# Kernel optimization log

Hardware: AMD Instinct MI355X
Metric: run time of the kernel (lower is better)

## Reference

```python
import jax, jax.numpy as jnp
import numpy as np

NATTRS, NOBJS = 200, 500
N = NATTRS + NOBJS
E = 50000
IN_F, HID, NODE_D = 512, 2048, 512
IMG_D, EMB = 512, 800
B = 256


def _ln(x, g, b, eps=1e-5):
    mu = jnp.mean(x, axis=-1, keepdims=True)
    var = jnp.mean((x - mu) ** 2, axis=-1, keepdims=True)
    return (x - mu) * jax.lax.rsqrt(var + eps) * g + b


def _sage(x, src, dst, Wl, bl, Wr):
    # PyG SAGEConv: lin_l(mean_{j->i} x_j) + lin_r(x_i); lin_r has no bias.
    agg = jax.ops.segment_sum(x[src], dst, num_segments=x.shape[0])
    cnt = jax.ops.segment_sum(jnp.ones((src.shape[0],), x.dtype), dst, num_segments=x.shape[0])
    mean = agg / jnp.maximum(cnt, 1.0)[:, None]
    return mean @ Wl + bl + x @ Wr


def setup_inputs() -> dict:
    key = jax.random.key(0)
    ks = iter(jax.random.split(key, 40))
    rn = lambda shape, s=0.02: jax.random.normal(next(ks), shape, jnp.float32) * s
    inp = dict(
        img=jax.random.normal(next(ks), (B, IMG_D), jnp.float32),
        node_feats=jax.random.normal(next(ks), (N, IN_F), jnp.float32),
        edge_index=jax.random.randint(next(ks), (2, E), 0, N),
        # SAGEConv 1: in_f -> 2048
        s1_Wl=rn((IN_F, HID)), s1_bl=jnp.zeros((HID,), jnp.float32), s1_Wr=rn((IN_F, HID)),
        # SAGEConv 2: 2048 -> node_dim
        s2_Wl=rn((HID, NODE_D)), s2_bl=jnp.zeros((NODE_D,), jnp.float32), s2_Wr=rn((HID, NODE_D)),
        # img_fc: 512 -> 800 -> 1000 -> 800 (LayerNorm+ReLU hidden, LayerNorm output)
        i_W1=rn((IMG_D, 800)), i_b1=jnp.zeros((800,), jnp.float32), i_g1=jnp.ones((800,), jnp.float32), i_be1=jnp.zeros((800,), jnp.float32),
        i_W2=rn((800, 1000)), i_b2=jnp.zeros((1000,), jnp.float32), i_g2=jnp.ones((1000,), jnp.float32), i_be2=jnp.zeros((1000,), jnp.float32),
        i_W3=rn((1000, EMB)), i_b3=jnp.zeros((EMB,), jnp.float32), i_gn=jnp.ones((EMB,), jnp.float32), i_bn=jnp.zeros((EMB,), jnp.float32),
        # pair_fc: 1024 -> 1000 -> 800
        p_W1=rn((2 * NODE_D, 1000)), p_b1=jnp.zeros((1000,), jnp.float32), p_g1=jnp.ones((1000,), jnp.float32), p_be1=jnp.zeros((1000,), jnp.float32),
        p_W2=rn((1000, EMB)), p_b2=jnp.zeros((EMB,), jnp.float32), p_gn=jnp.ones((EMB,), jnp.float32), p_bn=jnp.zeros((EMB,), jnp.float32),
    )
    return inp


def reference(img, node_feats, edge_index,
              s1_Wl, s1_bl, s1_Wr, s2_Wl, s2_bl, s2_Wr,
              i_W1, i_b1, i_g1, i_be1, i_W2, i_b2, i_g2, i_be2, i_W3, i_b3, i_gn, i_bn,
              p_W1, p_b1, p_g1, p_be1, p_W2, p_b2, p_gn, p_bn):
    src, dst = edge_index[0], edge_index[1]
    # GAE.encode: SAGE -> ReLU -> (Dropout, eval=id) -> SAGE
    h = jax.nn.relu(_sage(node_feats, src, dst, s1_Wl, s1_bl, s1_Wr))
    nodes = _sage(h, src, dst, s2_Wl, s2_bl, s2_Wr)  # [N, node_dim]
    # img_fc
    t = jax.nn.relu(_ln(img @ i_W1 + i_b1, i_g1, i_be1))
    t = jax.nn.relu(_ln(t @ i_W2 + i_b2, i_g2, i_be2))
    img_feats = _ln(t @ i_W3 + i_b3, i_gn, i_bn)  # [B, EMB]
    # get_all_pairs (open-world cross product: attr repeated per obj, obj tiled)
    attr_nodes, obj_nodes = nodes[:NATTRS], nodes[NATTRS:]
    pairs = jnp.concatenate(
        [jnp.repeat(attr_nodes, NOBJS, axis=0), jnp.tile(obj_nodes, (NATTRS, 1))], axis=1)  # [P, 2*node_dim]
    u = jax.nn.relu(_ln(pairs @ p_W1 + p_b1, p_g1, p_be1))
    pair_nodes = _ln(u @ p_W2 + p_b2, p_gn, p_bn)  # [P, EMB]
    pair_pred = img_feats @ pair_nodes.T  # [B, P]
    return pair_pred, nodes
```

## Files before the change

### kernel.cpp

```cpp
#include <hip/hip_runtime.h>
#include <hip/hip_bf16.h>

#define NATTRS 200
#define NOBJS  500
#define NNODE  700
#define IN_F   512
#define HID    2048
#define NODE_D 512
#define IMG_D  512
#define EMB    800
#define BB     256
#define P_H1   1000
#define NPAIR  100000

typedef __attribute__((ext_vector_type(8))) short short8v;
typedef __attribute__((ext_vector_type(4))) float f32x4;

typedef const __attribute__((address_space(1))) unsigned int* gas_ptr;
typedef __attribute__((address_space(3))) unsigned int* las_ptr;
__device__ __forceinline__ void async_copy16(void* lds, const void* g) {
  __builtin_amdgcn_global_load_lds((gas_ptr)g, (las_ptr)lds, 16, 0, 0);
}

__device__ __forceinline__ ushort f2bf(float x) {
  __hip_bfloat16 b = __float2bfloat16(x);
  return *reinterpret_cast<ushort*>(&b);
}
__device__ __forceinline__ float bf2f(ushort u) {
  __hip_bfloat16 b;
  *reinterpret_cast<ushort*>(&b) = u;
  return __bfloat162float(b);
}

__global__ void k_count(const int* __restrict__ ei, int* __restrict__ cnt, int E) {
  int e = blockIdx.x * 256 + threadIdx.x;
  if (e < E) atomicAdd(&cnt[ei[E + e]], 1);
}

__global__ __launch_bounds__(1024) void k_scan(const int* __restrict__ cnt,
                                               int* __restrict__ row_start,
                                               int* __restrict__ pos) {
  __shared__ int s[1024];
  int t = threadIdx.x;
  int my = (t < NNODE) ? cnt[t] : 0;
  s[t] = my;
  __syncthreads();
  for (int off = 1; off < 1024; off <<= 1) {
    int add = (t >= off) ? s[t - off] : 0;
    __syncthreads();
    s[t] += add;
    __syncthreads();
  }
  int excl = s[t] - my;
  if (t < NNODE) { row_start[t] = excl; pos[t] = excl; }
  if (t == 0) row_start[NNODE] = s[1023];
}

__global__ void k_fill(const int* __restrict__ ei, int* __restrict__ pos,
                       int* __restrict__ srcs, int E) {
  int e = blockIdx.x * 256 + threadIdx.x;
  if (e < E) {
    int d = ei[E + e];
    int idx = atomicAdd(&pos[d], 1);
    srcs[idx] = ei[e];
  }
}

__global__ __launch_bounds__(256) void agg_mean(const float* __restrict__ X,
                                                const int* __restrict__ srcs,
                                                const int* __restrict__ row_start,
                                                float* __restrict__ outp, int D) {
  int node = blockIdx.x;
  int d = blockIdx.y * 256 + threadIdx.x;
  int e0 = row_start[node], e1 = row_start[node + 1];
  float s = 0.f;
  for (int e = e0; e < e1; ++e) s += X[srcs[e] * D + d];
  float c = (float)(e1 - e0);
  outp[node * D + d] = s / fmaxf(c, 1.f);
}

__global__ __launch_bounds__(256) void split_f32(const float* __restrict__ X,
                                                 ushort* __restrict__ Xh,
                                                 ushort* __restrict__ Xl,
                                                 int Mvalid, int K, int Kpad, long total) {
  for (long idx = blockIdx.x * 256L + threadIdx.x; idx < total; idx += gridDim.x * 256L) {
    int m = (int)(idx / Kpad);
    int k = (int)(idx - (long)m * Kpad);
    float v = (m < Mvalid && k < K) ? X[(size_t)m * K + k] : 0.f;
    ushort h = f2bf(v);
    Xh[idx] = h;
    Xl[idx] = f2bf(v - bf2f(h));
  }
}

__global__ __launch_bounds__(256) void prep_wT(const float* __restrict__ W,
                                               ushort* __restrict__ Wh,
                                               ushort* __restrict__ Wl,
                                               int K, int N, int Kpad) {
  __shared__ float tile[32][33];
  const int n0 = blockIdx.x * 32, k0 = blockIdx.y * 32;
  const int tx = threadIdx.x & 31, ty = threadIdx.x >> 5;
  #pragma unroll
  for (int r0 = 0; r0 < 32; r0 += 8) {
    int k = k0 + r0 + ty, n = n0 + tx;
    tile[r0 + ty][tx] = (k < K && n < N) ? W[(size_t)k * N + n] : 0.f;
  }
  __syncthreads();
  #pragma unroll
  for (int r0 = 0; r0 < 32; r0 += 8) {
    int n = n0 + r0 + ty, kk = k0 + tx;
    float v = tile[tx][r0 + ty];
    ushort h = f2bf(v);
    Wh[(size_t)n * Kpad + kk] = h;
    Wl[(size_t)n * Kpad + kk] = f2bf(v - bf2f(h));
  }
}

template <bool RELU>
__global__ __launch_bounds__(256) void ln_rows(float* __restrict__ X,
                                               const float* __restrict__ g,
                                               const float* __restrict__ b, int N) {
  int row = blockIdx.x, tid = threadIdx.x;
  float* x = X + row * N;
  float s1 = 0.f, s2 = 0.f;
  for (int i = tid; i < N; i += 256) { float v = x[i]; s1 += v; s2 += v * v; }
  #pragma unroll
  for (int m = 1; m < 64; m <<= 1) { s1 += __shfl_xor(s1, m); s2 += __shfl_xor(s2, m); }
  __shared__ float r1[4], r2[4];
  int wv = tid >> 6;
  if ((tid & 63) == 0) { r1[wv] = s1; r2[wv] = s2; }
  __syncthreads();
  s1 = r1[0] + r1[1] + r1[2] + r1[3];
  s2 = r2[0] + r2[1] + r2[2] + r2[3];
  float inv = 1.f / (float)N;
  float mu = s1 * inv;
  float rstd = rsqrtf(s2 * inv - mu * mu + 1e-5f);
  for (int i = tid; i < N; i += 256) {
    float v = (x[i] - mu) * rstd * g[i] + b[i];
    if (RELU) v = fmaxf(v, 0.f);
    x[i] = v;
  }
}

__global__ __launch_bounds__(256) void prep_img(const float* __restrict__ t3,
                                                ushort* __restrict__ ih,
                                                ushort* __restrict__ il) {
  int r = blockIdx.x;
  for (int n = threadIdx.x; n < EMB; n += 256) {
    float v = t3[r * EMB + n];
    ushort h = f2bf(v);
    ih[r * EMB + n] = h;
    il[r * EMB + n] = f2bf(v - bf2f(h));
  }
}

__global__ __launch_bounds__(256) void ugen(const float* __restrict__ B1v,
                                            const float* __restrict__ O1v,
                                            const float* __restrict__ g1,
                                            const float* __restrict__ be1,
                                            ushort* __restrict__ Uh,
                                            ushort* __restrict__ Ul, int p0) {
  int r = blockIdx.x * 4 + (threadIdx.x >> 6);
  int lane = threadIdx.x & 63;
  int p = p0 + r;
  if (p > NPAIR - 1) p = NPAIR - 1;
  int a = p / NOBJS, o = p - a * NOBJS;
  const float* br = B1v + a * P_H1;
  const float* ow = O1v + o * P_H1;
  float x[16];
  float s1 = 0.f, s2 = 0.f;
  #pragma unroll
  for (int i = 0; i < 16; ++i) {
    int k = lane + 64 * i;
    float v = 0.f;
    if (k < P_H1) v = br[k] + ow[k];
    x[i] = v; s1 += v; s2 += v * v;
  }
  #pragma unroll
  for (int m = 1; m < 64; m <<= 1) { s1 += __shfl_xor(s1, m); s2 += __shfl_xor(s2, m); }
  float mu = s1 * (1.f / P_H1);
  float rstd = rsqrtf(s2 * (1.f / P_H1) - mu * mu + 1e-5f);
  size_t rb = (size_t)r * 1024;
  #pragma unroll
  for (int i = 0; i < 16; ++i) {
    int k = lane + 64 * i;
    float un = 0.f;
    if (k < P_H1) un = fmaxf((x[i] - mu) * rstd * g1[k] + be1[k], 0.f);
    ushort h = f2bf(un);
    Uh[rb + k] = h;
    Ul[rb + k] = f2bf(un - bf2f(h));
  }
}

__global__ __launch_bounds__(256) void ln2k(const float* __restrict__ Vr,
                                            const float* __restrict__ gn,
                                            const float* __restrict__ bn,
                                            ushort* __restrict__ Vh,
                                            ushort* __restrict__ Vl) {
  int r = blockIdx.x * 4 + (threadIdx.x >> 6);
  int lane = threadIdx.x & 63;
  const float* row = Vr + (size_t)r * EMB;
  float x[13];
  float s1 = 0.f, s2 = 0.f;
  #pragma unroll
  for (int i = 0; i < 13; ++i) {
    int k = lane + 64 * i;
    float v = (k < EMB) ? row[k] : 0.f;
    x[i] = v; s1 += v; s2 += v * v;
  }
  #pragma unroll
  for (int m = 1; m < 64; m <<= 1) { s1 += __shfl_xor(s1, m); s2 += __shfl_xor(s2, m); }
  float mu = s1 * (1.f / EMB);
  float rstd = rsqrtf(s2 * (1.f / EMB) - mu * mu + 1e-5f);
  size_t rb = (size_t)r * EMB;
  #pragma unroll
  for (int i = 0; i < 13; ++i) {
    int k = lane + 64 * i;
    if (k < EMB) {
      float v = (x[i] - mu) * rstd * gn[k] + bn[k];
      ushort h = f2bf(v);
      Vh[rb + k] = h;
      Vl[rb + k] = f2bf(v - bf2f(h));
    }
  }
}

template <bool HAS2, bool HASBIAS, bool RELU>
__global__ __launch_bounds__(256, 3) void gemm_mf(
    const ushort* __restrict__ Ah, const ushort* __restrict__ Al, int lda,
    const ushort* __restrict__ Bh, const ushort* __restrict__ Bl, int ldb,
    const ushort* __restrict__ A2h, const ushort* __restrict__ A2l, int lda2,
    const ushort* __restrict__ B2h, const ushort* __restrict__ B2l, int ldb2,
    const float* __restrict__ bias, float* __restrict__ C, size_t ldc,
    int K, int Mvalid, int nvalid, int ncol0) {
  __shared__ ushort smem[16384];
  const int tid = threadIdx.x, lane = tid & 63, wid = tid >> 6;
  const int wm = wid >> 1, wn = wid & 1;
  const int n0b = blockIdx.x * 128, m0 = blockIdx.y * 128;
  const int lr = lane & 15, lk = lane >> 4;

  f32x4 acc[4][4];
  #pragma unroll
  for (int i = 0; i < 4; ++i)
    #pragma unroll
    for (int j = 0; j < 4; ++j) acc[i][j] = (f32x4){0.f, 0.f, 0.f, 0.f};

  const int srow = lane >> 2;
  const int scol = (lane & 3) * 8;
  const int npass = HAS2 ? 2 : 1;

  for (int pass = 0; pass < npass; ++pass) {
    const ushort* pAh = (HAS2 && pass) ? A2h : Ah;
    const ushort* pAl = (HAS2 && pass) ? A2l : Al;
    const ushort* pBh = (HAS2 && pass) ? B2h : Bh;
    const ushort* pBl = (HAS2 && pass) ? B2l : Bl;
    const int plda = (HAS2 && pass) ? lda2 : lda;
    const int pldb = (HAS2 && pass) ? ldb2 : ldb;

    for (int k0 = 0; k0 < K; k0 += 32) {
      __syncthreads();
      #pragma unroll
      for (int j = 0; j < 8; ++j) {
        int t = wid + 4 * j;
        int buf = t >> 3, i = t & 7;
        const ushort* g;
        int ld_, r0;
        if (buf == 0)      { g = pAh; ld_ = plda; r0 = m0; }
        else if (buf == 1) { g = pAl; ld_ = plda; r0 = m0; }
        else if (buf == 2) { g = pBh; ld_ = pldb; r0 = n0b; }
        else               { g = pBl; ld_ = pldb; r0 = n0b; }
        const ushort* src = g + (size_t)(r0 + i * 16 + srow) * ld_ + k0 + scol;
        async_copy16(smem + buf * 4096 + i * 512, src);
      }
      __syncthreads();

      short8v ah[4], al[4], bh[4], bl[4];
      #pragma unroll
      for (int f = 0; f < 4; ++f) {
        ah[f] = *(const short8v*)&smem[0     + (wm * 64 + f * 16 + lr) * 32 + lk * 8];
        al[f] = *(const short8v*)&smem[4096  + (wm * 64 + f * 16 + lr) * 32 + lk * 8];
        bh[f] = *(const short8v*)&smem[8192  + (wn * 64 + f * 16 + lr) * 32 + lk * 8];
        bl[f] = *(const short8v*)&smem[12288 + (wn * 64 + f * 16 + lr) * 32 + lk * 8];
      }
      #pragma unroll
      for (int mi = 0; mi < 4; ++mi)
        #pragma unroll
        for (int ni = 0; ni < 4; ++ni) {
          acc[mi][ni] = __builtin_amdgcn_mfma_f32_16x16x32_bf16(ah[mi], bh[ni], acc[mi][ni], 0, 0, 0);
          acc[mi][ni] = __builtin_amdgcn_mfma_f32_16x16x32_bf16(al[mi], bh[ni], acc[mi][ni], 0, 0, 0);
          acc[mi][ni] = __builtin_amdgcn_mfma_f32_16x16x32_bf16(ah[mi], bl[ni], acc[mi][ni], 0, 0, 0);
        }
    }
  }

  #pragma unroll
  for (int mi = 0; mi < 4; ++mi)
    #pragma unroll
    for (int ni = 0; ni < 4; ++ni) {
      #pragma unroll
      for (int r = 0; r < 4; ++r) {
        int m = m0 + wm * 64 + mi * 16 + lk * 4 + r;
        int n = n0b + wn * 64 + ni * 16 + lr;
        if (m < Mvalid && n < nvalid) {
          float v = acc[mi][ni][r];
          if (HASBIAS) v += bias[n];
          if (RELU) v = fmaxf(v, 0.f);
          C[(size_t)m * ldc + ncol0 + n] = v;
        }
      }
    }
}

extern "C" void kernel_launch(void* const* d_in, const int* in_sizes, int n_in,
                              void* d_out, int out_size, void* d_ws, size_t ws_size,
                              hipStream_t stream) {
  const float* img = (const float*)d_in[0];
  const float* node_feats = (const float*)d_in[1];
  const int* ei = (const int*)d_in[2];
  const float* s1_Wl = (const float*)d_in[3];
  const float* s1_bl = (const float*)d_in[4];
  const float* s1_Wr = (const float*)d_in[5];
  const float* s2_Wl = (const float*)d_in[6];
  const float* s2_bl = (const float*)d_in[7];
  const float* s2_Wr = (const float*)d_in[8];
  const float* i_W1 = (const float*)d_in[9];
  const float* i_b1 = (const float*)d_in[10];
  const float* i_g1 = (const float*)d_in[11];
  const float* i_be1 = (const float*)d_in[12];
  const float* i_W2 = (const float*)d_in[13];
  const float* i_b2 = (const float*)d_in[14];
  const float* i_g2 = (const float*)d_in[15];
  const float* i_be2 = (const float*)d_in[16];
  const float* i_W3 = (const float*)d_in[17];
  const float* i_b3 = (const float*)d_in[18];
  const float* i_gn = (const float*)d_in[19];
  const float* i_bn = (const float*)d_in[20];
  const float* p_W1 = (const float*)d_in[21];
  const float* p_b1 = (const float*)d_in[22];
  const float* p_g1 = (const float*)d_in[23];
  const float* p_be1 = (const float*)d_in[24];
  const float* p_W2 = (const float*)d_in[25];
  const float* p_b2 = (const float*)d_in[26];
  const float* p_gn = (const float*)d_in[27];
  const float* p_bn = (const float*)d_in[28];

  const int E = in_sizes[2] / 2;

  char* base = (char*)d_ws;
  size_t off = 0;
  auto alloc = [&](size_t bytes) -> void* {
    void* p = base + off;
    off = (off + bytes + 255) & ~(size_t)255;
    return p;
  };
  float* mean1 = (float*)alloc(700 * 512 * 4);
  float* h     = (float*)alloc(700 * 2048 * 4);
  float* mean2 = (float*)alloc(700 * 2048 * 4);
  float* t1    = (float*)alloc(256 * 800 * 4);
  float* t2    = (float*)alloc(256 * 1000 * 4);
  float* t3    = (float*)alloc(256 * 800 * 4);
  float* B1    = (float*)alloc(200 * 1000 * 4);
  float* O1    = (float*)alloc(500 * 1000 * 4);
  ushort* nfh = (ushort*)alloc(768 * 512 * 2);
  ushort* nfl = (ushort*)alloc(768 * 512 * 2);
  ushort* m1h = (ushort*)alloc(768 * 512 * 2);
  ushort* m1l = (ushort*)alloc(768 * 512 * 2);
  ushort* hh  = (ushort*)alloc(768 * 2048 * 2);
  ushort* hl  = (ushort*)alloc(768 * 2048 * 2);
  ushort* m2h = (ushort*)alloc(768 * 2048 * 2);
  ushort* m2l = (ushort*)alloc(768 * 2048 * 2);
  ushort* ndh = (ushort*)alloc(768 * 512 * 2);
  ushort* ndl = (ushort*)alloc(768 * 512 * 2);
  ushort* xih = (ushort*)alloc(256 * 512 * 2);
  ushort* xil = (ushort*)alloc(256 * 512 * 2);
  ushort* t1h = (ushort*)alloc(256 * 800 * 2);
  ushort* t1l = (ushort*)alloc(256 * 800 * 2);
  ushort* t2h = (ushort*)alloc(256 * 1024 * 2);
  ushort* t2l = (ushort*)alloc(256 * 1024 * 2);
  ushort* imgh = (ushort*)alloc(256 * 800 * 2);
  ushort* imgl = (ushort*)alloc(256 * 800 * 2);
  ushort* w1lh = (ushort*)alloc((size_t)2048 * 512 * 2);
  ushort* w1ll = (ushort*)alloc((size_t)2048 * 512 * 2);
  ushort* w1rh = (ushort*)alloc((size_t)2048 * 512 * 2);
  ushort* w1rl = (ushort*)alloc((size_t)2048 * 512 * 2);
  ushort* w2lh = (ushort*)alloc((size_t)512 * 2048 * 2);
  ushort* w2ll = (ushort*)alloc((size_t)512 * 2048 * 2);
  ushort* w2rh = (ushort*)alloc((size_t)512 * 2048 * 2);
  ushort* w2rl = (ushort*)alloc((size_t)512 * 2048 * 2);
  ushort* iw1h = (ushort*)alloc((size_t)896 * 512 * 2);
  ushort* iw1l = (ushort*)alloc((size_t)896 * 512 * 2);
  ushort* iw2h = (ushort*)alloc((size_t)1024 * 800 * 2);
  ushort* iw2l = (ushort*)alloc((size_t)1024 * 800 * 2);
  ushort* iw3h = (ushort*)alloc((size_t)896 * 1024 * 2);
  ushort* iw3l = (ushort*)alloc((size_t)896 * 1024 * 2);
  ushort* pw1ah = (ushort*)alloc((size_t)1024 * 512 * 2);
  ushort* pw1al = (ushort*)alloc((size_t)1024 * 512 * 2);
  ushort* pw1bh = (ushort*)alloc((size_t)1024 * 512 * 2);
  ushort* pw1bl = (ushort*)alloc((size_t)1024 * 512 * 2);
  ushort* W2Th = (ushort*)alloc((size_t)896 * 1024 * 2);
  ushort* W2Tl = (ushort*)alloc((size_t)896 * 1024 * 2);
  int* cnt       = (int*)alloc(704 * 4);
  int* row_start = (int*)alloc(704 * 4);
  int* pos       = (int*)alloc(704 * 4);
  int* srcs      = (int*)alloc(50176 * 4);

  size_t avail = (ws_size > off + (4u << 20)) ? ws_size - off - (4u << 20) : 0;
  long maxRows = (long)(avail / 10496) - 128;
  int CA = (int)(maxRows / 500);
  if (CA < 1) CA = 1;
  if (CA > 50) CA = 50;
  int nch = (NATTRS + CA - 1) / CA;
  int rowsPadAlloc = ((CA * 500 + 127) / 128) * 128;
  ushort* Uh   = (ushort*)alloc((size_t)rowsPadAlloc * 1024 * 2);
  ushort* Ul   = (ushort*)alloc((size_t)rowsPadAlloc * 1024 * 2);
  float*  Vraw = (float*) alloc((size_t)rowsPadAlloc * 800 * 4);
  ushort* Vh   = (ushort*)alloc((size_t)rowsPadAlloc * 800 * 2);
  ushort* Vl   = (ushort*)alloc((size_t)rowsPadAlloc * 800 * 2);

  float* pairp = (float*)d_out;
  float* nodes = (float*)d_out + (size_t)BB * NPAIR;

  const ushort* NU = nullptr;

  hipMemsetAsync(cnt, 0, NNODE * sizeof(int), stream);
  k_count<<<(E + 255) / 256, 256, 0, stream>>>(ei, cnt, E);
  k_scan<<<1, 1024, 0, stream>>>(cnt, row_start, pos);
  k_fill<<<(E + 255) / 256, 256, 0, stream>>>(ei, pos, srcs, E);

  prep_wT<<<dim3(2048 / 32, 512 / 32), 256, 0, stream>>>(s1_Wl, w1lh, w1ll, 512, 2048, 512);
  prep_wT<<<dim3(2048 / 32, 512 / 32), 256, 0, stream>>>(s1_Wr, w1rh, w1rl, 512, 2048, 512);
  prep_wT<<<dim3(512 / 32, 2048 / 32), 256, 0, stream>>>(s2_Wl, w2lh, w2ll, 2048, 512, 2048);
  prep_wT<<<dim3(512 / 32, 2048 / 32), 256, 0, stream>>>(s2_Wr, w2rh, w2rl, 2048, 512, 2048);
  prep_wT<<<dim3(896 / 32, 512 / 32), 256, 0, stream>>>(i_W1, iw1h, iw1l, 512, 800, 512);
  prep_wT<<<dim3(1024 / 32, 800 / 32), 256, 0, stream>>>(i_W2, iw2h, iw2l, 800, 1000, 800);
  prep_wT<<<dim3(896 / 32, 1024 / 32), 256, 0, stream>>>(i_W3, iw3h, iw3l, 1000, 800, 1024);
  prep_wT<<<dim3(1024 / 32, 512 / 32), 256, 0, stream>>>(p_W1, pw1ah, pw1al, 512, 1000, 512);
  prep_wT<<<dim3(1024 / 32, 512 / 32), 256, 0, stream>>>(p_W1 + 512 * 1000, pw1bh, pw1bl, 512, 1000, 512);
  prep_wT<<<dim3(896 / 32, 1024 / 32), 256, 0, stream>>>(p_W2, W2Th, W2Tl, 1000, 800, 1024);

  agg_mean<<<dim3(NNODE, IN_F / 256), 256, 0, stream>>>(node_feats, srcs, row_start, mean1, IN_F);
  split_f32<<<512, 256, 0, stream>>>(node_feats, nfh, nfl, 700, 512, 512, 768L * 512);
  split_f32<<<512, 256, 0, stream>>>(mean1, m1h, m1l, 700, 512, 512, 768L * 512);
  gemm_mf<true, true, true><<<dim3(16, 6), 256, 0, stream>>>(
      m1h, m1l, 512, w1lh, w1ll, 512, nfh, nfl, 512, w1rh, w1rl, 512,
      s1_bl, h, 2048, 512, 700, 2048, 0);

  agg_mean<<<dim3(NNODE, HID / 256), 256, 0, stream>>>(h, srcs, row_start, mean2, HID);
  split_f32<<<1024, 256, 0, stream>>>(h, hh, hl, 700, 2048, 2048, 768L * 2048);
  split_f32<<<1024, 256, 0, stream>>>(mean2, m2h, m2l, 700, 2048, 2048, 768L * 2048);
  gemm_mf<true, true, false><<<dim3(4, 6), 256, 0, stream>>>(
      m2h, m2l, 2048, w2lh, w2ll, 2048, hh, hl, 2048, w2rh, w2rl, 2048,
      s2_bl, nodes, 512, 2048, 700, 512, 0);

  split_f32<<<256, 256, 0, stream>>>(img, xih, xil, 256, 512, 512, 256L * 512);
  gemm_mf<false, true, false><<<dim3(7, 2), 256, 0, stream>>>(
      xih, xil, 512, iw1h, iw1l, 512, NU, NU, 0, NU, NU, 0,
      i_b1, t1, 800, 512, 256, 800, 0);
  ln_rows<true><<<BB, 256, 0, stream>>>(t1, i_g1, i_be1, 800);
  split_f32<<<256, 256, 0, stream>>>(t1, t1h, t1l, 256, 800, 800, 256L * 800);
  gemm_mf<false, true, false><<<dim3(8, 2), 256, 0, stream>>>(
      t1h, t1l, 800, iw2h, iw2l, 800, NU, NU, 0, NU, NU, 0,
      i_b2, t2, 1000, 800, 256, 1000, 0);
  ln_rows<true><<<BB, 256, 0, stream>>>(t2, i_g2, i_be2, 1000);
  split_f32<<<256, 256, 0, stream>>>(t2, t2h, t2l, 256, 1000, 1024, 256L * 1024);
  gemm_mf<false, true, false><<<dim3(7, 2), 256, 0, stream>>>(
      t2h, t2l, 1024, iw3h, iw3l, 1024, NU, NU, 0, NU, NU, 0,
      i_b3, t3, 800, 1024, 256, 800, 0);
  ln_rows<false><<<BB, 256, 0, stream>>>(t3, i_gn, i_bn, EMB);
  prep_img<<<BB, 256, 0, stream>>>(t3, imgh, imgl);

  split_f32<<<512, 256, 0, stream>>>(nodes, ndh, ndl, 700, 512, 512, 768L * 512);
  gemm_mf<false, true, false><<<dim3(8, 2), 256, 0, stream>>>(
      ndh, ndl, 512, pw1ah, pw1al, 512, NU, NU, 0, NU, NU, 0,
      p_b1, B1, 1000, 512, 200, 1000, 0);
  gemm_mf<false, false, false><<<dim3(8, 4), 256, 0, stream>>>(
      ndh + 200 * 512, ndl + 200 * 512, 512, pw1bh, pw1bl, 512, NU, NU, 0, NU, NU, 0,
      nullptr, O1, 1000, 512, 500, 1000, 0);

  for (int c = 0; c < nch; ++c) {
    int a0 = c * CA;
    int ca = (NATTRS - a0 < CA) ? (NATTRS - a0) : CA;
    int rows = ca * 500;
    int rowsPad = ((rows + 127) / 128) * 128;
    int p0 = a0 * 500;

    ugen<<<rowsPad / 4, 256, 0, stream>>>(B1, O1, p_g1, p_be1, Uh, Ul, p0);
    gemm_mf<false, true, false><<<dim3(7, rowsPad / 128), 256, 0, stream>>>(
        Uh, Ul, 1024, W2Th, W2Tl, 1024, NU, NU, 0, NU, NU, 0,
        p_b2, Vraw, 800, 1024, rowsPad, 800, 0);
    ln2k<<<rowsPad / 4, 256, 0, stream>>>(Vraw, p_gn, p_bn, Vh, Vl);
    gemm_mf<false, false, false><<<dim3(rowsPad / 128, 2), 256, 0, stream>>>(
        imgh, imgl, 800, Vh, Vl, 800, NU, NU, 0, NU, NU, 0,
        nullptr, pairp, NPAIR, 800, 256, rows, p0);
  }
}
```

Measured before the change: 1.892 ms.

## Fold pair LayerNorm into final GEMM via precomputed img·W2 projection

Rewrites pair_pred = img_feats·LN(U·W2+b2)ᵀ algebraically as rstd·(G·Uᵀ + img·b2 − mu·S) + T, with G = (img⊙gn)·W2ᵀ precomputed once. The full [P,800] V materialisation and its separate LayerNorm kernel are dropped. Per-row mean and rstd now come from a lightweight ustat kernel that recomputes U·W2 using only the bf16-high part, plus an extra W2 rowsum column for the mean. The ten weight-transpose launches are batched into one kernel, ugen gets vectorised stores, and chunk sizing changes because less workspace is needed. The risks are precision loss in the variance (single-bf16 statistics, E[x²]−mu² cancellation) and the ustat GEMM still repeating the big matmul work.

```diff
diff --git a/kernel.cpp b/kernel.cpp
--- a/kernel.cpp
+++ b/kernel.cpp
@@ -93,17 +93,24 @@
   }
 }
 
-__global__ __launch_bounds__(256) void prep_wT(const float* __restrict__ W,
-                                               ushort* __restrict__ Wh,
-                                               ushort* __restrict__ Wl,
-                                               int K, int N, int Kpad) {
+struct WDesc { const float* W; ushort* Wh; ushort* Wl; int K, N, Kpad, nbx, blk0; };
+struct WBatch { WDesc d[10]; };
+
+__global__ __launch_bounds__(256) void prep_wT_batch(WBatch B) {
   __shared__ float tile[32][33];
-  const int n0 = blockIdx.x * 32, k0 = blockIdx.y * 32;
+  int bx = blockIdx.x;
+  int di = 0;
+  #pragma unroll
+  for (int j = 1; j < 10; ++j) if (bx >= B.d[j].blk0) di = j;
+  const WDesc& D = B.d[di];
+  int local = bx - D.blk0;
+  int bn = local % D.nbx, bk = local / D.nbx;
+  const int n0 = bn * 32, k0 = bk * 32;
   const int tx = threadIdx.x & 31, ty = threadIdx.x >> 5;
   #pragma unroll
   for (int r0 = 0; r0 < 32; r0 += 8) {
     int k = k0 + r0 + ty, n = n0 + tx;
-    tile[r0 + ty][tx] = (k < K && n < N) ? W[(size_t)k * N + n] : 0.f;
+    tile[r0 + ty][tx] = (k < D.K && n < D.N) ? D.W[(size_t)k * D.N + n] : 0.f;
   }
   __syncthreads();
   #pragma unroll
@@ -111,9 +118,21 @@
     int n = n0 + r0 + ty, kk = k0 + tx;
     float v = tile[tx][r0 + ty];
     ushort h = f2bf(v);
-    Wh[(size_t)n * Kpad + kk] = h;
-    Wl[(size_t)n * Kpad + kk] = f2bf(v - bf2f(h));
-  }
+    D.Wh[(size_t)n * D.Kpad + kk] = h;
+    D.Wl[(size_t)n * D.Kpad + kk] = f2bf(v - bf2f(h));
+  }
+}
+
+__global__ __launch_bounds__(256) void w2rowsum(const float* __restrict__ W2,
+                                                ushort* __restrict__ W2Th) {
+  int k = blockIdx.x * 4 + (threadIdx.x >> 6);
+  int lane = threadIdx.x & 63;
+  const float* row = W2 + (size_t)k * EMB;
+  float s = 0.f;
+  for (int n = lane; n < EMB; n += 64) s += row[n];
+  #pragma unroll
+  for (int m = 1; m < 64; m <<= 1) s += __shfl_xor(s, m);
+  if (lane == 0 && k < P_H1) W2Th[800 * 1024 + k] = f2bf(s);
 }
 
 template <bool RELU>
@@ -142,15 +161,54 @@
   }
 }
 
-__global__ __launch_bounds__(256) void prep_img(const float* __restrict__ t3,
-                                                ushort* __restrict__ ih,
-                                                ushort* __restrict__ il) {
+__global__ __launch_bounds__(256) void prep_imgg(const float* __restrict__ t3,
+                                                 const float* __restrict__ gn,
+                                                 ushort* __restrict__ gh,
+                                                 ushort* __restrict__ gl) {
   int r = blockIdx.x;
   for (int n = threadIdx.x; n < EMB; n += 256) {
-    float v = t3[r * EMB + n];
+    float v = t3[r * EMB + n] * gn[n];
     ushort h = f2bf(v);
-    ih[r * EMB + n] = h;
-    il[r * EMB + n] = f2bf(v - bf2f(h));
+    gh[r * EMB + n] = h;
+    gl[r * EMB + n] = f2bf(v - bf2f(h));
+  }
+}
+
+__global__ __launch_bounds__(256) void prep_pairB(const float* __restrict__ t3,
+                                                  const float* __restrict__ gn,
+                                                  const float* __restrict__ bn,
+                                                  const float* __restrict__ b2,
+                                                  float* __restrict__ Sv, float* __restrict__ Tv,
+                                                  float* __restrict__ IBv, float* __restrict__ aux) {
+  int b = blockIdx.x, tid = threadIdx.x;
+  __shared__ float r1[4], r2[4], r3[4];
+  float s1 = 0.f, s2 = 0.f, s3 = 0.f;
+  if (b == BB) {
+    for (int n = tid; n < EMB; n += 256) s1 += b2[n];
+    #pragma unroll
+    for (int m = 1; m < 64; m <<= 1) s1 += __shfl_xor(s1, m);
+    if ((tid & 63) == 0) r1[tid >> 6] = s1;
+    __syncthreads();
+    if (tid == 0) aux[0] = (r1[0] + r1[1] + r1[2] + r1[3]) * (1.f / EMB);
+    return;
+  }
+  const float* row = t3 + b * EMB;
+  for (int n = tid; n < EMB; n += 256) {
+    float iv = row[n];
+    float ig = iv * gn[n];
+    s1 += ig; s2 += iv * bn[n]; s3 += ig * b2[n];
+  }
+  #pragma unroll
+  for (int m = 1; m < 64; m <<= 1) {
+    s1 += __shfl_xor(s1, m); s2 += __shfl_xor(s2, m); s3 += __shfl_xor(s3, m);
+  }
+  int wv = tid >> 6;
+  if ((tid & 63) == 0) { r1[wv] = s1; r2[wv] = s2; r3[wv] = s3; }
+  __syncthreads();
+  if (tid == 0) {
+    Sv[b] = r1[0] + r1[1] + r1[2] + r1[3];
+    Tv[b] = r2[0] + r2[1] + r2[2] + r2[3];
+    IBv[b] = r3[0] + r3[1] + r3[2] + r3[3];
   }
 }
 
@@ -167,72 +225,147 @@
   int a = p / NOBJS, o = p - a * NOBJS;
   const float* br = B1v + a * P_H1;
   const float* ow = O1v + o * P_H1;
+  const int kb = lane * 16;
   float x[16];
   float s1 = 0.f, s2 = 0.f;
   #pragma unroll
   for (int i = 0; i < 16; ++i) {
-    int k = lane + 64 * i;
-    float v = 0.f;
-    if (k < P_H1) v = br[k] + ow[k];
+    int k = kb + i;
+    float v = (k < P_H1) ? br[k] + ow[k] : 0.f;
     x[i] = v; s1 += v; s2 += v * v;
   }
   #pragma unroll
   for (int m = 1; m < 64; m <<= 1) { s1 += __shfl_xor(s1, m); s2 += __shfl_xor(s2, m); }
   float mu = s1 * (1.f / P_H1);
   float rstd = rsqrtf(s2 * (1.f / P_H1) - mu * mu + 1e-5f);
-  size_t rb = (size_t)r * 1024;
+  ushort hv[16], lv[16];
   #pragma unroll
   for (int i = 0; i < 16; ++i) {
-    int k = lane + 64 * i;
-    float un = 0.f;
-    if (k < P_H1) un = fmaxf((x[i] - mu) * rstd * g1[k] + be1[k], 0.f);
+    int k = kb + i;
+    float un = (k < P_H1) ? fmaxf((x[i] - mu) * rstd * g1[k] + be1[k], 0.f) : 0.f;
     ushort h = f2bf(un);
-    Uh[rb + k] = h;
-    Ul[rb + k] = f2bf(un - bf2f(h));
-  }
-}
-
-__global__ __launch_bounds__(256) void ln2k(const float* __restrict__ Vr,
-                                            const float* __restrict__ gn,
-                                            const float* __restrict__ bn,
-                                            ushort* __restrict__ Vh,
-                                            ushort* __restrict__ Vl) {
-  int r = blockIdx.x * 4 + (threadIdx.x >> 6);
-  int lane = threadIdx.x & 63;
-  const float* row = Vr + (size_t)r * EMB;
-  float x[13];
-  float s1 = 0.f, s2 = 0.f;
-  #pragma unroll
-  for (int i = 0; i < 13; ++i) {
-    int k = lane + 64 * i;
-    float v = (k < EMB) ? row[k] : 0.f;
-    x[i] = v; s1 += v; s2 += v * v;
-  }
-  #pragma unroll
-  for (int m = 1; m < 64; m <<= 1) { s1 += __shfl_xor(s1, m); s2 += __shfl_xor(s2, m); }
-  float mu = s1 * (1.f / EMB);
-  float rstd = rsqrtf(s2 * (1.f / EMB) - mu * mu + 1e-5f);
-  size_t rb = (size_t)r * EMB;
-  #pragma unroll
-  for (int i = 0; i < 13; ++i) {
-    int k = lane + 64 * i;
-    if (k < EMB) {
-      float v = (x[i] - mu) * rstd * gn[k] + bn[k];
-      ushort h = f2bf(v);
-      Vh[rb + k] = h;
-      Vl[rb + k] = f2bf(v - bf2f(h));
+    hv[i] = h;
+    lv[i] = f2bf(un - bf2f(h));
+  }
+  size_t base = (size_t)r * 1024 + kb;
+  *(short8v*)&Uh[base] = *(short8v*)&hv[0];
+  *(short8v*)&Uh[base + 8] = *(short8v*)&hv[8];
+  *(short8v*)&Ul[base] = *(short8v*)&lv[0];
+  *(short8v*)&Ul[base + 8] = *(short8v*)&lv[8];
+}
+
+__global__ __launch_bounds__(256, 3) void ustat(const ushort* __restrict__ Uh,
+                                                const ushort* __restrict__ W2Th,
+                                                const float* __restrict__ b2,
+                                                const float* __restrict__ aux,
+                                                float* __restrict__ muv,
+                                                float* __restrict__ rstdv) {
+  __shared__ ushort smem[8192];
+  __shared__ float red[2][128];
+  const int tid = threadIdx.x, lane = tid & 63, wid = tid >> 6;
+  const int wm = wid >> 1, wn = wid & 1;
+  const int m0 = blockIdx.x * 128;
+  const int lr = lane & 15, lk = lane >> 4;
+  const int srow = lane >> 2;
+  const int scol = (lane & 3) * 8;
+  const float aux0 = aux[0];
+
+  float ss[4][4] = {};
+  float md[4][4] = {};
+
+  for (int nt = 0; nt < 7; ++nt) {
+    f32x4 acc[4][4];
+    #pragma unroll
+    for (int i = 0; i < 4; ++i)
+      #pragma unroll
+      for (int j = 0; j < 4; ++j) acc[i][j] = (f32x4){0.f, 0.f, 0.f, 0.f};
+
+    for (int k0 = 0; k0 < 1024; k0 += 32) {
+      __syncthreads();
+      #pragma unroll
+      for (int j = 0; j < 4; ++j) {
+        int t = wid + 4 * j;
+        int buf = t >> 3, i = t & 7;
+        const ushort* src = buf == 0
+            ? Uh + (size_t)(m0 + i * 16 + srow) * 1024 + k0 + scol
+            : W2Th + (size_t)(nt * 128 + i * 16 + srow) * 1024 + k0 + scol;
+        async_copy16(smem + buf * 4096 + i * 512, src);
+      }
+      __syncthreads();
+      short8v ah[4], bh[4];
+      #pragma unroll
+      for (int f = 0; f < 4; ++f) {
+        ah[f] = *(const short8v*)&smem[(wm * 64 + f * 16 + lr) * 32 + lk * 8];
+        bh[f] = *(const short8v*)&smem[4096 + (wn * 64 + f * 16 + lr) * 32 + lk * 8];
+      }
+      #pragma unroll
+      for (int mi = 0; mi < 4; ++mi)
+        #pragma unroll
+        for (int ni = 0; ni < 4; ++ni)
+          acc[mi][ni] = __builtin_amdgcn_mfma_f32_16x16x32_bf16(ah[mi], bh[ni], acc[mi][ni], 0, 0, 0);
     }
-  }
-}
-
-template <bool HAS2, bool HASBIAS, bool RELU>
+    #pragma unroll
+    for (int ni = 0; ni < 4; ++ni) {
+      int n = nt * 128 + wn * 64 + ni * 16 + lr;
+      if (n < EMB) {
+        float bb = b2[n];
+        #pragma unroll
+        for (int mi = 0; mi < 4; ++mi)
+          #pragma unroll
+          for (int r = 0; r < 4; ++r) {
+            float v = acc[mi][ni][r] + bb;
+            ss[mi][r] += v * v;
+          }
+      } else if (n == EMB) {
+        #pragma unroll
+        for (int mi = 0; mi < 4; ++mi)
+          #pragma unroll
+          for (int r = 0; r < 4; ++r) md[mi][r] = acc[mi][ni][r];
+      }
+    }
+  }
+  #pragma unroll
+  for (int mi = 0; mi < 4; ++mi)
+    #pragma unroll
+    for (int r = 0; r < 4; ++r) {
+      float s = ss[mi][r];
+      s += __shfl_xor(s, 1); s += __shfl_xor(s, 2);
+      s += __shfl_xor(s, 4); s += __shfl_xor(s, 8);
+      ss[mi][r] = s;
+    }
+  if (lr == 0) {
+    #pragma unroll
+    for (int mi = 0; mi < 4; ++mi)
+      #pragma unroll
+      for (int r = 0; r < 4; ++r)
+        red[wn][wm * 64 + mi * 16 + lk * 4 + r] = ss[mi][r];
+  }
+  __syncthreads();
+  if (wn == 0 && lr == 0) {
+    #pragma unroll
+    for (int mi = 0; mi < 4; ++mi)
+      #pragma unroll
+      for (int r = 0; r < 4; ++r) {
+        int row = wm * 64 + mi * 16 + lk * 4 + r;
+        float tot = red[0][row] + red[1][row];
+        float m_ = md[mi][r] * (1.f / EMB) + aux0;
+        muv[m0 + row] = m_;
+        rstdv[m0 + row] = rsqrtf(tot * (1.f / EMB) - m_ * m_ + 1e-5f);
+      }
+  }
+}
+
+template <bool HAS2, bool HASBIAS, bool RELU, bool PAIREPI>
 __global__ __launch_bounds__(256, 3) void gemm_mf(
     const ushort* __restrict__ Ah, const ushort* __restrict__ Al, int lda,
     const ushort* __restrict__ Bh, const ushort* __restrict__ Bl, int ldb,
     const ushort* __restrict__ A2h, const ushort* __restrict__ A2l, int lda2,
     const ushort* __restrict__ B2h, const ushort* __restrict__ B2l, int ldb2,
     const float* __restrict__ bias, float* __restrict__ C, size_t ldc,
-    int K, int Mvalid, int nvalid, int ncol0) {
+    int K, int Mvalid, int nvalid, int ncol0,
+    const float* __restrict__ rstdv, const float* __restrict__ muv,
+    const float* __restrict__ Sv, const float* __restrict__ Tv,
+    const float* __restrict__ IBv) {
   __shared__ ushort smem[16384];
   const int tid = threadIdx.x, lane = tid & 63, wid = tid >> 6;
   const int wm = wid >> 1, wn = wid & 1;
@@ -297,16 +430,23 @@
   for (int mi = 0; mi < 4; ++mi)
     #pragma unroll
     for (int ni = 0; ni < 4; ++ni) {
+      int n = n0b + wn * 64 + ni * 16 + lr;
+      if (n >= nvalid) continue;
+      float rs = 0.f, mn = 0.f;
+      if (PAIREPI) { rs = rstdv[n]; mn = muv[n]; }
+      float bb = (HASBIAS && !PAIREPI) ? bias[n] : 0.f;
       #pragma unroll
       for (int r = 0; r < 4; ++r) {
         int m = m0 + wm * 64 + mi * 16 + lk * 4 + r;
-        int n = n0b + wn * 64 + ni * 16 + lr;
-        if (m < Mvalid && n < nvalid) {
-          float v = acc[mi][ni][r];
-          if (HASBIAS) v += bias[n];
+        if (m >= Mvalid) continue;
+        float v = acc[mi][ni][r];
+        if (PAIREPI) {
+          v = rs * (v + IBv[m] - mn * Sv[m]) + Tv[m];
+        } else {
+          v += bb;
           if (RELU) v = fmaxf(v, 0.f);
-          C[(size_t)m * ldc + ncol0 + n] = v;
         }
+        C[(size_t)m * ldc + ncol0 + n] = v;
       }
     }
 }
@@ -361,6 +501,7 @@
   float* t3    = (float*)alloc(256 * 800 * 4);
   float* B1    = (float*)alloc(200 * 1000 * 4);
   float* O1    = (float*)alloc(500 * 1000 * 4);
+  float* G     = (float*)alloc(256 * 1024 * 4);
   ushort* nfh = (ushort*)alloc(768 * 512 * 2);
   ushort* nfl = (ushort*)alloc(768 * 512 * 2);
   ushort* m1h = (ushort*)alloc(768 * 512 * 2);
@@ -377,8 +518,10 @@
   ushort* t1l = (ushort*)alloc(256 * 800 * 2);
   ushort* t2h = (ushort*)alloc(256 * 1024 * 2);
   ushort* t2l = (ushort*)alloc(256 * 1024 * 2);
-  ushort* imgh = (ushort*)alloc(256 * 800 * 2);
-  ushort* imgl = (ushort*)alloc(256 * 800 * 2);
+  ushort* iggh = (ushort*)alloc(256 * 800 * 2);
+  ushort* iggl = (ushort*)alloc(256 * 800 * 2);
+  ushort* Gh   = (ushort*)alloc(256 * 1024 * 2);
+  ushort* Gl   = (ushort*)alloc(256 * 1024 * 2);
   ushort* w1lh = (ushort*)alloc((size_t)2048 * 512 * 2);
   ushort* w1ll = (ushort*)alloc((size_t)2048 * 512 * 2);
   ushort* w1rh = (ushort*)alloc((size_t)2048 * 512 * 2);
@@ -399,83 +542,106 @@
   ushort* pw1bl = (ushort*)alloc((size_t)1024 * 512 * 2);
   ushort* W2Th = (ushort*)alloc((size_t)896 * 1024 * 2);
   ushort* W2Tl = (ushort*)alloc((size_t)896 * 1024 * 2);
+  ushort* Wkh  = (ushort*)alloc((size_t)1024 * 800 * 2);
+  ushort* Wkl  = (ushort*)alloc((size_t)1024 * 800 * 2);
+  float* Sv  = (float*)alloc(256 * 4);
+  float* Tv  = (float*)alloc(256 * 4);
+  float* IBv = (float*)alloc(256 * 4);
+  float* aux = (float*)alloc(256);
   int* cnt       = (int*)alloc(704 * 4);
   int* row_start = (int*)alloc(704 * 4);
   int* pos       = (int*)alloc(704 * 4);
   int* srcs      = (int*)alloc(50176 * 4);
 
   size_t avail = (ws_size > off + (4u << 20)) ? ws_size - off - (4u << 20) : 0;
-  long maxRows = (long)(avail / 10496) - 128;
+  long maxRows = (long)(avail / 4104) - 256;
   int CA = (int)(maxRows / 500);
   if (CA < 1) CA = 1;
-  if (CA > 50) CA = 50;
+  if (CA > NATTRS) CA = NATTRS;
   int nch = (NATTRS + CA - 1) / CA;
   int rowsPadAlloc = ((CA * 500 + 127) / 128) * 128;
-  ushort* Uh   = (ushort*)alloc((size_t)rowsPadAlloc * 1024 * 2);
-  ushort* Ul   = (ushort*)alloc((size_t)rowsPadAlloc * 1024 * 2);
-  float*  Vraw = (float*) alloc((size_t)rowsPadAlloc * 800 * 4);
-  ushort* Vh   = (ushort*)alloc((size_t)rowsPadAlloc * 800 * 2);
-  ushort* Vl   = (ushort*)alloc((size_t)rowsPadAlloc * 800 * 2);
+  ushort* Uh    = (ushort*)alloc((size_t)rowsPadAlloc * 1024 * 2);
+  ushort* Ul    = (ushort*)alloc((size_t)rowsPadAlloc * 1024 * 2);
+  float*  muv   = (float*)alloc((size_t)rowsPadAlloc * 4);
+  float*  rstdv = (float*)alloc((size_t)rowsPadAlloc * 4);
 
   float* pairp = (float*)d_out;
   float* nodes = (float*)d_out + (size_t)BB * NPAIR;
 
   const ushort* NU = nullptr;
+  const float* NUF = nullptr;
 
   hipMemsetAsync(cnt, 0, NNODE * sizeof(int), stream);
   k_count<<<(E + 255) / 256, 256, 0, stream>>>(ei, cnt, E);
   k_scan<<<1, 1024, 0, stream>>>(cnt, row_start, pos);
   k_fill<<<(E + 255) / 256, 256, 0, stream>>>(ei, pos, srcs, E);
 
-  prep_wT<<<dim3(2048 / 32, 512 / 32), 256, 0, stream>>>(s1_Wl, w1lh, w1ll, 512, 2048, 512);
-  prep_wT<<<dim3(2048 / 32, 512 / 32), 256, 0, stream>>>(s1_Wr, w1rh, w1rl, 512, 2048, 512);
-  prep_wT<<<dim3(512 / 32, 2048 / 32), 256, 0, stream>>>(s2_Wl, w2lh, w2ll, 2048, 512, 2048);
-  prep_wT<<<dim3(512 / 32, 2048 / 32), 256, 0, stream>>>(s2_Wr, w2rh, w2rl, 2048, 512, 2048);
-  prep_wT<<<dim3(896 / 32, 512 / 32), 256, 0, stream>>>(i_W1, iw1h, iw1l, 512, 800, 512);
-  prep_wT<<<dim3(1024 / 32, 800 / 32), 256, 0, stream>>>(i_W2, iw2h, iw2l, 800, 1000, 800);
-  prep_wT<<<dim3(896 / 32, 1024 / 32), 256, 0, stream>>>(i_W3, iw3h, iw3l, 1000, 800, 1024);
-  prep_wT<<<dim3(1024 / 32, 512 / 32), 256, 0, stream>>>(p_W1, pw1ah, pw1al, 512, 1000, 512);
-  prep_wT<<<dim3(1024 / 32, 512 / 32), 256, 0, stream>>>(p_W1 + 512 * 1000, pw1bh, pw1bl, 512, 1000, 512);
-  prep_wT<<<dim3(896 / 32, 1024 / 32), 256, 0, stream>>>(p_W2, W2Th, W2Tl, 1000, 800, 1024);
+  {
+    WBatch B;
+    int blk = 0;
+    auto set = [&](int i, const float* W, ushort* Wh, ushort* Wl, int K, int N, int Kpad, int Npad) {
+      B.d[i] = {W, Wh, Wl, K, N, Kpad, Npad / 32, blk};
+      blk += (Npad / 32) * (Kpad / 32);
+    };
+    set(0, s1_Wl, w1lh, w1ll, 512, 2048, 512, 2048);
+    set(1, s1_Wr, w1rh, w1rl, 512, 2048, 512, 2048);
+    set(2, s2_Wl, w2lh, w2ll, 2048, 512, 2048, 512);
+    set(3, s2_Wr, w2rh, w2rl, 2048, 512, 2048, 512);
+    set(4, i_W1, iw1h, iw1l, 512, 800, 512, 896);
+    set(5, i_W2, iw2h, iw2l, 800, 1000, 800, 1024);
+    set(6, i_W3, iw3h, iw3l, 1000, 800, 1024, 896);
+    set(7, p_W1, pw1ah, pw1al, 512, 1000, 512, 1024);
+    set(8, p_W1 + 512 * 1000, pw1bh, pw1bl, 512, 1000, 512, 1024);
+    set(9, p_W2, W2Th, W2Tl, 1000, 800, 1024, 896);
+    prep_wT_batch<<<blk, 256, 0, stream>>>(B);
+  }
+  w2rowsum<<<250, 256, 0, stream>>>(p_W2, W2Th);
+  split_f32<<<512, 256, 0, stream>>>(p_W2, Wkh, Wkl, 1000, 800, 800, 1024L * 800);
 
   agg_mean<<<dim3(NNODE, IN_F / 256), 256, 0, stream>>>(node_feats, srcs, row_start, mean1, IN_F);
   split_f32<<<512, 256, 0, stream>>>(node_feats, nfh, nfl, 700, 512, 512, 768L * 512);
   split_f32<<<512, 256, 0, stream>>>(mean1, m1h, m1l, 700, 512, 512, 768L * 512);
-  gemm_mf<true, true, true><<<dim3(16, 6), 256, 0, stream>>>(
+  gemm_mf<true, true, true, false><<<dim3(16, 6), 256, 0, stream>>>(
       m1h, m1l, 512, w1lh, w1ll, 512, nfh, nfl, 512, w1rh, w1rl, 512,
-      s1_bl, h, 2048, 512, 700, 2048, 0);
+      s1_bl, h, 2048, 512, 700, 2048, 0, NUF, NUF, NUF, NUF, NUF);
 
   agg_mean<<<dim3(NNODE, HID / 256), 256, 0, stream>>>(h, srcs, row_start, mean2, HID);
   split_f32<<<1024, 256, 0, stream>>>(h, hh, hl, 700, 2048, 2048, 768L * 2048);
   split_f32<<<1024, 256, 0, stream>>>(mean2, m2h, m2l, 700, 2048, 2048, 768L * 2048);
-  gemm_mf<true, true, false><<<dim3(4, 6), 256, 0, stream>>>(
+  gemm_mf<true, true, false, false><<<dim3(4, 6), 256, 0, stream>>>(
       m2h, m2l, 2048, w2lh, w2ll, 2048, hh, hl, 2048, w2rh, w2rl, 2048,
-      s2_bl, nodes, 512, 2048, 700, 512, 0);
+      s2_bl, nodes, 512, 2048, 700, 512, 0, NUF, NUF, NUF, NUF, NUF);
 
   split_f32<<<256, 256, 0, stream>>>(img, xih, xil, 256, 512, 512, 256L * 512);
-  gemm_mf<false, true, false><<<dim3(7, 2), 256, 0, stream>>>(
+  gemm_mf<false, true, false, false><<<dim3(7, 2), 256, 0, stream>>>(
       xih, xil, 512, iw1h, iw1l, 512, NU, NU, 0, NU, NU, 0,
-      i_b1, t1, 800, 512, 256, 800, 0);
+      i_b1, t1, 800, 512, 256, 800, 0, NUF, NUF, NUF, NUF, NUF);
   ln_rows<true><<<BB, 256, 0, stream>>>(t1, i_g1, i_be1, 800);
   split_f32<<<256, 256, 0, stream>>>(t1, t1h, t1l, 256, 800, 800, 256L * 800);
-  gemm_mf<false, true, false><<<dim3(8, 2), 256, 0, stream>>>(
+  gemm_mf<false, true, false, false><<<dim3(8, 2), 256, 0, stream>>>(
       t1h, t1l, 800, iw2h, iw2l, 800, NU, NU, 0, NU, NU, 0,
-      i_b2, t2, 1000, 800, 256, 1000, 0);
+      i_b2, t2, 1000, 800, 256, 1000, 0, NUF, NUF, NUF, NUF, NUF);
   ln_rows<true><<<BB, 256, 0, stream>>>(t2, i_g2, i_be2, 1000);
   split_f32<<<256, 256, 0, stream>>>(t2, t2h, t2l, 256, 1000, 1024, 256L * 1024);
-  gemm_mf<false, true, false><<<dim3(7, 2), 256, 0, stream>>>(
+  gemm_mf<false, true, false, false><<<dim3(7, 2), 256, 0, stream>>>(
       t2h, t2l, 1024, iw3h, iw3l, 1024, NU, NU, 0, NU, NU, 0,
-      i_b3, t3, 800, 1024, 256, 800, 0);
+      i_b3, t3, 800, 1024, 256, 800, 0, NUF, NUF, NUF, NUF, NUF);
   ln_rows<false><<<BB, 256, 0, stream>>>(t3, i_gn, i_bn, EMB);
-  prep_img<<<BB, 256, 0, stream>>>(t3, imgh, imgl);
+
+  prep_pairB<<<BB + 1, 256, 0, stream>>>(t3, p_gn, p_bn, p_b2, Sv, Tv, IBv, aux);
+  prep_imgg<<<BB, 256, 0, stream>>>(t3, p_gn, iggh, iggl);
+  gemm_mf<false, false, false, false><<<dim3(8, 2), 256, 0, stream>>>(
+      iggh, iggl, 800, Wkh, Wkl, 800, NU, NU, 0, NU, NU, 0,
+      nullptr, G, 1024, 800, 256, 1024, 0, NUF, NUF, NUF, NUF, NUF);
+  split_f32<<<256, 256, 0, stream>>>(G, Gh, Gl, 256, 1024, 1024, 256L * 1024);
 
   split_f32<<<512, 256, 0, stream>>>(nodes, ndh, ndl, 700, 512, 512, 768L * 512);
-  gemm_mf<false, true, false><<<dim3(8, 2), 256, 0, stream>>>(
+  gemm_mf<false, true, false, false><<<dim3(8, 2), 256, 0, stream>>>(
       ndh, ndl, 512, pw1ah, pw1al, 512, NU, NU, 0, NU, NU, 0,
-      p_b1, B1, 1000, 512, 200, 1000, 0);
-  gemm_mf<false, false, false><<<dim3(8, 4), 256, 0, stream>>>(
+      p_b1, B1, 1000, 512, 200, 1000, 0, NUF, NUF, NUF, NUF, NUF);
+  gemm_mf<false, false, false, false><<<dim3(8, 4), 256, 0, stream>>>(
       ndh + 200 * 512, ndl + 200 * 512, 512, pw1bh, pw1bl, 512, NU, NU, 0, NU, NU, 0,
-      nullptr, O1, 1000, 512, 500, 1000, 0);
+      nullptr, O1, 1000, 512, 500, 1000, 0, NUF, NUF, NUF, NUF, NUF);
 
   for (int c = 0; c < nch; ++c) {
     int a0 = c * CA;
@@ -485,12 +651,10 @@
     int p0 = a0 * 500;
 
     ugen<<<rowsPad / 4, 256, 0, stream>>>(B1, O1, p_g1, p_be1, Uh, Ul, p0);
-    gemm_mf<false, true, false><<<dim3(7, rowsPad / 128), 256, 0, stream>>>(
-        Uh, Ul, 1024, W2Th, W2Tl, 1024, NU, NU, 0, NU, NU, 0,
-        p_b2, Vraw, 800, 1024, rowsPad, 800, 0);
-    ln2k<<<rowsPad / 4, 256, 0, stream>>>(Vraw, p_gn, p_bn, Vh, Vl);
-    gemm_mf<false, false, false><<<dim3(rowsPad / 128, 2), 256, 0, stream>>>(
-        imgh, imgl, 800, Vh, Vl, 800, NU, NU, 0, NU, NU, 0,
-        nullptr, pairp, NPAIR, 800, 256, rows, p0);
-  }
-}
+    ustat<<<rowsPad / 128, 256, 0, stream>>>(Uh, W2Th, p_b2, aux, muv, rstdv);
+    gemm_mf<false, false, false, true><<<dim3(rowsPad / 128, 2), 256, 0, stream>>>(
+        Gh, Gl, 1024, Uh, Ul, 1024, NU, NU, 0, NU, NU, 0,
+        nullptr, pairp, NPAIR, 1024, 256, rows, p0,
+        rstdv, muv, Sv, Tv, IBv);
+  }
+}
```

Result: slower. 2.134 ms (+12.8%).
